# Performance work log

Hardware: AMD Instinct MI355X
Metric: run time of the kernel (lower is better)

## Reference

```python
import jax, jax.numpy as jnp
import numpy as np
from jax import lax

D_MODEL = 2048
D_STATE = 16
D_CONV = 4
B_SZ = 2
T_LEN = 2048


def setup_inputs() -> dict:
    key = jax.random.key(0)
    ks = jax.random.split(key, 8)
    x = jax.random.normal(ks[0], (B_SZ, T_LEN, D_MODEL), dtype=jnp.float32)
    h = jnp.zeros((B_SZ, D_MODEL, D_STATE), dtype=jnp.float32)
    norm_w = jnp.ones((D_MODEL,), dtype=jnp.float32)
    in_proj_w = jax.random.normal(ks[1], (2 * D_MODEL, D_MODEL), dtype=jnp.float32) * (D_MODEL ** -0.5)
    conv_w = jax.random.normal(ks[2], (D_MODEL, 1, D_CONV), dtype=jnp.float32) * 0.5
    conv_b = jnp.zeros((D_MODEL,), dtype=jnp.float32)
    x_proj_w = jax.random.normal(ks[3], (D_MODEL + 2 * D_STATE, D_MODEL), dtype=jnp.float32) * (D_MODEL ** -0.5)
    A_log = jnp.broadcast_to(jnp.log(jnp.arange(1, D_STATE + 1, dtype=jnp.float32))[None, :], (D_MODEL, D_STATE)).copy()
    D = jnp.ones((D_MODEL,), dtype=jnp.float32)
    out_proj_w = jax.random.normal(ks[4], (D_MODEL, D_MODEL), dtype=jnp.float32) * (D_MODEL ** -0.5)
    return {"x": x, "h": h, "norm_w": norm_w, "in_proj_w": in_proj_w,
            "conv_w": conv_w, "conv_b": conv_b, "x_proj_w": x_proj_w,
            "A_log": A_log, "D": D, "out_proj_w": out_proj_w}


def _rmsnorm(x, w, eps=1e-6):
    ms = jnp.mean(jnp.square(x.astype(jnp.float32)), axis=-1, keepdims=True)
    return (x * lax.rsqrt(ms + eps).astype(x.dtype)) * w.astype(x.dtype)


def reference(x, h, norm_w, in_proj_w, conv_w, conv_b, x_proj_w, A_log, D, out_proj_w):
    B, T, d_model = x.shape
    d_state = A_log.shape[1]
    residual = x
    x_normed = _rmsnorm(x, norm_w)
    xz = x_normed @ in_proj_w.T                      # (B, T, 2*d_model)
    x_branch, z = jnp.split(xz, 2, axis=-1)
    # depthwise causal conv1d: torch pads both sides by d_conv-1 then slices [:T],
    # equivalent to left-pad-only causal conv.
    xc = x_branch.transpose(0, 2, 1)                 # (B, d_model, T)
    xc = lax.conv_general_dilated(
        xc, conv_w, window_strides=(1,), padding=[(D_CONV - 1, 0)],
        dimension_numbers=("NCH", "OIH", "NCH"), feature_group_count=d_model)
    xc = xc + conv_b[None, :, None]
    x_ssm = jax.nn.silu(xc.transpose(0, 2, 1))       # (B, T, d_model)

    # SSM core
    proj = x_ssm @ x_proj_w.T                        # (B, T, d_model + 2*d_state)
    delta_raw = proj[..., :d_model]
    B_in = proj[..., d_model:d_model + d_state]
    C_in = proj[..., d_model + d_state:]
    delta = jax.nn.softplus(delta_raw)               # (B, T, d_model)
    A = -jnp.exp(A_log.astype(jnp.float32))          # (d_model, d_state)

    def step(h_c, inp):
        d_t, b_t, c_t, x_t = inp                     # (B,dm) (B,ds) (B,ds) (B,dm)
        A_bar = jnp.exp(d_t[:, :, None] * A[None])   # (B, dm, ds)
        h_c = A_bar * h_c + (d_t * x_t)[:, :, None] * b_t[:, None, :]
        y_t = jnp.einsum("bdn,bn->bd", h_c, c_t) + D * x_t
        return h_c, y_t

    xs = (delta.transpose(1, 0, 2), B_in.transpose(1, 0, 2),
          C_in.transpose(1, 0, 2), x_ssm.transpose(1, 0, 2))
    h_new, ys = lax.scan(step, h.astype(x.dtype), xs)
    y = ys.transpose(1, 0, 2)                        # (B, T, d_model)

    y = y * jax.nn.silu(z)
    out = residual + y @ out_proj_w.T
    return out, lax.stop_gradient(h_new)
```

## Files before the change

kernel.cpp:

```cpp
#include <hip/hip_runtime.h>
#include <cstdint>
#include <cstddef>


typedef __bf16 bf16_t;
typedef __attribute__((ext_vector_type(8))) __bf16 bf16x8;
typedef __attribute__((ext_vector_type(4))) __bf16 bf16x4;
typedef __attribute__((ext_vector_type(4))) float f32x4;

#define D_MODEL 2048
#define D_STATE 16
#define B_SZ 2
#define T_LEN 2048
#define N_ROWS (B_SZ * T_LEN)
#define N_PAD  2304
#define N_CHUNK 32
#define L_CHUNK (T_LEN / N_CHUNK)
#define LOG2E 1.4426950408889634f

__device__ __forceinline__ void load_lds16(const void* g, void* l) {
    __builtin_amdgcn_global_load_lds(
        (const __attribute__((address_space(1))) void*)(uintptr_t)g,
        (__attribute__((address_space(3))) void*)(uintptr_t)l,
        16, 0, 0);
}

#define VMW(n) asm volatile("s_waitcnt vmcnt(" #n ")" ::: "memory")
#define BAR()  do { __builtin_amdgcn_s_barrier(); __builtin_amdgcn_sched_barrier(0); } while (0)

__global__ __launch_bounds__(256) void cast_w13(
    const float* __restrict__ w1, const float* __restrict__ w3,
    bf16_t* __restrict__ d1, bf16_t* __restrict__ d3)
{
    int i = blockIdx.x * 256 + threadIdx.x;
    const int n1 = 4096 * 2048 / 4;
    if (i < n1) {
        f32x4 v = ((const f32x4*)w1)[i];
        ((bf16x4*)d1)[i] = __builtin_convertvector(v, bf16x4);
    } else {
        int j = i - n1;
        f32x4 v = ((const f32x4*)w3)[j];
        ((bf16x4*)d3)[j] = __builtin_convertvector(v, bf16x4);
    }
}

__global__ __launch_bounds__(256) void cast_pad_w2(
    const float* __restrict__ s, bf16_t* __restrict__ d)
{
    int i = blockIdx.x * 256 + threadIdx.x;
    int row = i >> 11;
    int col = i & 2047;
    float v = (row < 2080) ? s[(size_t)row * 2048 + col] : 0.f;
    d[i] = (bf16_t)v;
}

__global__ __launch_bounds__(256) void rmsnorm_kernel(
    const float* __restrict__ x, const float* __restrict__ w,
    bf16_t* __restrict__ xn)
{
    int row = blockIdx.x;
    int tid = threadIdx.x;
    const f32x4* xr = (const f32x4*)(x + (size_t)row * D_MODEL);
    f32x4 v0 = xr[tid];
    f32x4 v1 = xr[tid + 256];
    float ss = 0.f;
    #pragma unroll
    for (int e = 0; e < 4; ++e) { ss = fmaf(v0[e], v0[e], ss); ss = fmaf(v1[e], v1[e], ss); }
    #pragma unroll
    for (int o = 32; o > 0; o >>= 1) ss += __shfl_down(ss, o, 64);
    __shared__ float red[4];
    if ((tid & 63) == 0) red[tid >> 6] = ss;
    __syncthreads();
    float tot = red[0] + red[1] + red[2] + red[3];
    float scale = rsqrtf(tot * (1.f / D_MODEL) + 1e-6f);
    const f32x4* w4 = (const f32x4*)w;
    f32x4 m0 = v0 * w4[tid] * scale;
    f32x4 m1 = v1 * w4[tid + 256] * scale;
    bf16x4* xo = (bf16x4*)(xn + (size_t)row * D_MODEL);
    xo[tid]       = __builtin_convertvector(m0, bf16x4);
    xo[tid + 256] = __builtin_convertvector(m1, bf16x4);
}

template<int MODE>
__global__ __launch_bounds__(512, 2) void gemm_bt(
    const bf16_t* __restrict__ A, const bf16_t* __restrict__ Bw, int K,
    float* __restrict__ out0, bf16_t* __restrict__ out1,
    const float* __restrict__ add)
{
    __shared__ __align__(16) char smem[131072];
    char* const ldsAp = smem;
    char* const ldsBp = smem + 32768;

    const int tid  = threadIdx.x;
    const int nwg = gridDim.x * gridDim.y;
    const int lin = blockIdx.x + gridDim.x * blockIdx.y;
    const int wg  = (lin & 7) * (nwg >> 3) + (lin >> 3);
    const int bm  = wg & 15;
    const int bn  = wg >> 4;

    const int lane = tid & 63;
    const int wave = tid >> 6;
    const int wm   = wave >> 2;
    const int wn   = wave & 3;
    const int fr   = lane & 15;
    const int quad = lane >> 4;

    const int rS   = tid >> 2;
    const int cS   = tid & 3;
    const int gcol = ((cS - ((rS >> 1) & 3)) & 3) * 8;
    const bf16_t* pAg = A  + (size_t)(bm * 256 + rS) * K + gcol;
    const bf16_t* pBg = Bw + (size_t)(bn * 256 + rS) * K + gcol;

    const int swz  = ((quad + ((fr >> 1) & 3)) & 3) * 8;
    const int aOff = (wm * 128 + fr) * 32 + swz;
    const int bOff = (wn * 64  + fr) * 32 + swz;

    f32x4 acc[8][4];
    #pragma unroll
    for (int i = 0; i < 8; ++i)
        #pragma unroll
        for (int j = 0; j < 4; ++j) acc[i][j] = {0.f, 0.f, 0.f, 0.f};

    bf16x8 bfr[4];

#define STG_A(b, t, s) do { \
        const bf16_t* g_ = pAg + (t) * 64 + (s) * 32; \
        char* l_ = ldsAp + (b) * 65536 + (s) * 16384 + tid * 16; \
        load_lds16(g_, l_); load_lds16(g_ + (size_t)128 * K, l_ + 8192); } while (0)
#define STG_B(b, t, s) do { \
        const bf16_t* g_ = pBg + (t) * 64 + (s) * 32; \
        char* l_ = ldsBp + (b) * 65536 + (s) * 16384 + tid * 16; \
        load_lds16(g_, l_); load_lds16(g_ + (size_t)128 * K, l_ + 8192); } while (0)

#define PHASE(BUF, S, IH, STAGE_STMT, TAIL_STMT)                              \
    {                                                                         \
        const bf16_t* pA_ = (const bf16_t*)(ldsAp + (BUF)*65536 + (S)*16384); \
        if ((IH) == 0) {                                                      \
            const bf16_t* pB_ =                                               \
                (const bf16_t*)(ldsBp + (BUF)*65536 + (S)*16384);             \
            _Pragma("unroll")                                                 \
            for (int j = 0; j < 4; ++j)                                       \
                bfr[j] = *(const bf16x8*)(pB_ + bOff + j * 512);              \
        }                                                                     \
        bf16x8 af0 = *(const bf16x8*)(pA_ + aOff + ((IH)*4 + 0) * 512);       \
        bf16x8 af1 = *(const bf16x8*)(pA_ + aOff + ((IH)*4 + 1) * 512);       \
        bf16x8 af2 = *(const bf16x8*)(pA_ + aOff + ((IH)*4 + 2) * 512);       \
        bf16x8 af3 = *(const bf16x8*)(pA_ + aOff + ((IH)*4 + 3) * 512);       \
        STAGE_STMT;                                                           \
        BAR();                                                                \
        __builtin_amdgcn_s_setprio(1);                                        \
        _Pragma("unroll")                                                     \
        for (int j = 0; j < 4; ++j)                                           \
            acc[(IH)*4+0][j] = __builtin_amdgcn_mfma_f32_16x16x32_bf16(       \
                af0, bfr[j], acc[(IH)*4+0][j], 0, 0, 0);                      \
        _Pragma("unroll")                                                     \
        for (int j = 0; j < 4; ++j)                                           \
            acc[(IH)*4+1][j] = __builtin_amdgcn_mfma_f32_16x16x32_bf16(       \
                af1, bfr[j], acc[(IH)*4+1][j], 0, 0, 0);                      \
        _Pragma("unroll")                                                     \
        for (int j = 0; j < 4; ++j)                                           \
            acc[(IH)*4+2][j] = __builtin_amdgcn_mfma_f32_16x16x32_bf16(       \
                af2, bfr[j], acc[(IH)*4+2][j], 0, 0, 0);                      \
        _Pragma("unroll")                                                     \
        for (int j = 0; j < 4; ++j)                                           \
            acc[(IH)*4+3][j] = __builtin_amdgcn_mfma_f32_16x16x32_bf16(       \
                af3, bfr[j], acc[(IH)*4+3][j], 0, 0, 0);                      \
        __builtin_amdgcn_s_setprio(0);                                        \
        TAIL_STMT;                                                            \
        BAR();                                                                \
    }

    STG_B(0, 0, 0); STG_A(0, 0, 0); STG_B(0, 0, 1); STG_A(0, 0, 1);
    STG_B(1, 1, 0); STG_A(1, 1, 0); STG_B(1, 1, 1);
    VMW(10); BAR();

    const int NI = K >> 7;
    for (int I = 0; I < NI - 1; ++I) {
        const int t2 = 2 * I + 2, t3 = 2 * I + 3;
        PHASE(0, 0, 0, STG_A(1, t2 - 1, 1), (void)0)
        PHASE(0, 0, 1, STG_B(0, t2, 0),     VMW(10))
        PHASE(0, 1, 0, STG_A(0, t2, 0),     (void)0)
        PHASE(0, 1, 1, STG_B(0, t2, 1),     VMW(10))
        PHASE(1, 0, 0, STG_A(0, t2, 1),     (void)0)
        PHASE(1, 0, 1, STG_B(1, t3, 0),     VMW(10))
        PHASE(1, 1, 0, STG_A(1, t3, 0),     (void)0)
        PHASE(1, 1, 1, STG_B(1, t3, 1),     VMW(10))
    }
    PHASE(0, 0, 0, STG_A(1, 2 * NI - 1, 1), (void)0)
    PHASE(0, 0, 1, (void)0, VMW(8))
    PHASE(0, 1, 0, (void)0, (void)0)
    PHASE(0, 1, 1, (void)0, VMW(4))
    PHASE(1, 0, 0, (void)0, (void)0)
    PHASE(1, 0, 1, (void)0, VMW(0))
    PHASE(1, 1, 0, (void)0, (void)0)
    PHASE(1, 1, 1, (void)0, (void)0)
#undef STG_A
#undef STG_B
#undef PHASE

    float* const cs = (float*)smem;
    __syncthreads();
    #pragma unroll
    for (int s = 0; s < 4; ++s) {
        if (wm == (s >> 1)) {
            #pragma unroll
            for (int ii = 0; ii < 4; ++ii)
                #pragma unroll
                for (int j = 0; j < 4; ++j)
                    #pragma unroll
                    for (int rr = 0; rr < 4; ++rr)
                        cs[(ii * 16 + quad * 4 + rr) * 268 + wn * 64 + j * 16 + fr]
                            = acc[(s & 1) * 4 + ii][j][rr];
        }
        __syncthreads();
        #pragma unroll
        for (int k = 0; k < 8; ++k) {
            const int idx = tid + k * 512;
            const int row = idx >> 6;
            const int c4  = (idx & 63) << 2;
            f32x4 v = *(const f32x4*)(cs + row * 268 + c4);
            const int gr = bm * 256 + s * 64 + row;
            const int gc = bn * 256 + c4;
            if (MODE == 0) {
                if (bn < 8) {
                    *(f32x4*)&out0[(size_t)gr * 2048 + gc] = v;
                } else {
                    bf16x4 o;
                    #pragma unroll
                    for (int e = 0; e < 4; ++e) {
                        float sv = v[e];
                        o[e] = (bf16_t)(sv / (1.f + __expf(-sv)));
                    }
                    *(bf16x4*)&out1[(size_t)gr * 2048 + (gc - 2048)] = o;
                }
            } else if (MODE == 1) {
                if (bn < 8) {
                    #pragma unroll
                    for (int e = 0; e < 4; ++e) {
                        float sv = v[e];
                        v[e] = fmaxf(sv, 0.f) + __logf(1.f + __expf(-fabsf(sv)));
                    }
                }
                *(f32x4*)&out0[(size_t)gr * N_PAD + gc] = v;
            } else {
                f32x4 a4 = *(const f32x4*)&add[(size_t)gr * 2048 + gc];
                *(f32x4*)&out0[(size_t)gr * 2048 + gc] = v + a4;
            }
        }
        __syncthreads();
    }
}

__global__ __launch_bounds__(256) void conv_silu_kernel(
    const float* __restrict__ xb, const float* __restrict__ cw,
    const float* __restrict__ cb, bf16_t* __restrict__ xs_b)
{
    int id = blockIdx.x * 256 + threadIdx.x;
    int d  = id & 2047;
    int tb = (id >> 11) & 255;
    int b  = id >> 19;
    float w0 = cw[d * 4 + 0], w1 = cw[d * 4 + 1], w2 = cw[d * 4 + 2], w3 = cw[d * 4 + 3];
    float bias = cb[d];
    int t0 = tb * 8;
    size_t base = (size_t)b * T_LEN;
    float v[11];
    #pragma unroll
    for (int i = 0; i < 11; ++i) {
        int t = t0 - 3 + i;
        v[i] = (t >= 0) ? xb[(base + t) * 2048 + d] : 0.f;
    }
    #pragma unroll
    for (int j = 0; j < 8; ++j) {
        float s = bias + w0 * v[j] + w1 * v[j + 1] + w2 * v[j + 2] + w3 * v[j + 3];
        float sl = s / (1.f + __expf(-s));
        xs_b[(base + t0 + j) * D_MODEL + d] = (bf16_t)sl;
    }
}

#define PF 4

__global__ __launch_bounds__(256) void scan_phase1(
    const float* __restrict__ proj, const bf16_t* __restrict__ xs,
    const float* __restrict__ A_log,
    float* __restrict__ Aprod, float* __restrict__ hfin)
{
    int wi   = blockIdx.x * 4 + (threadIdx.x >> 6);
    int lane = threadIdx.x & 63;
    int nq   = lane & 3;
    int dsub = lane >> 2;
    int c  = wi & 31;
    int dg = (wi >> 5) & 127;
    int b  = wi >> 12;
    int dd = dg * 16 + dsub;

    float A2[4], h[4], Ap[4];
    #pragma unroll
    for (int j = 0; j < 4; ++j) {
        A2[j] = -__expf(A_log[dd * D_STATE + nq * 4 + j]) * LOG2E;
        h[j] = 0.f; Ap[j] = 1.f;
    }
    const int t0 = c * L_CHUNK;
    const int tmax = t0 + L_CHUNK - 1;

    float p_da[PF], p_xv[PF];
    f32x4 p_B[PF];
    #pragma unroll
    for (int u = 0; u < PF; ++u) {
        size_t row = (size_t)b * T_LEN + t0 + u;
        const float* pr = proj + row * N_PAD;
        p_da[u] = pr[dd];
        p_xv[u] = (float)xs[row * D_MODEL + dd];
        p_B[u]  = *(const f32x4*)(pr + D_MODEL + nq * 4);
    }

    for (int it = 0; it < L_CHUNK; it += PF) {
        #pragma unroll
        for (int u = 0; u < PF; ++u) {
            int t = t0 + it + u;
            float da = p_da[u], xv = p_xv[u];
            f32x4 Bv = p_B[u];
            int tn = t + PF; tn = (tn > tmax) ? tmax : tn;
            {
                size_t row = (size_t)b * T_LEN + tn;
                const float* pr = proj + row * N_PAD;
                p_da[u] = pr[dd];
                p_xv[u] = (float)xs[row * D_MODEL + dd];
                p_B[u]  = *(const f32x4*)(pr + D_MODEL + nq * 4);
            }
            float dx = da * xv;
            #pragma unroll
            for (int j = 0; j < 4; ++j) {
                float a = exp2f(da * A2[j]);
                Ap[j] *= a;
                h[j] = fmaf(a, h[j], dx * Bv[j]);
            }
        }
    }
    size_t o = ((size_t)c * 4096 + b * 2048 + dd) * D_STATE + nq * 4;
    *(f32x4*)(Aprod + o) = f32x4{Ap[0], Ap[1], Ap[2], Ap[3]};
    *(f32x4*)(hfin  + o) = f32x4{h[0], h[1], h[2], h[3]};
}

__global__ __launch_bounds__(256) void scan_phase2(
    const float* __restrict__ h_in, const float* __restrict__ Aprod,
    float* __restrict__ hfin, float* __restrict__ h_out)
{
    int g = blockIdx.x * 256 + threadIdx.x;
    float h = h_in[g];
    for (int c = 0; c < N_CHUNK; ++c) {
        size_t o = (size_t)c * 65536 + g;
        float a   = Aprod[o];
        float loc = hfin[o];
        hfin[o] = h;
        h = fmaf(a, h, loc);
    }
    h_out[g] = h;
}

__global__ __launch_bounds__(256) void scan_phase3(
    const float* __restrict__ proj, const bf16_t* __restrict__ xs,
    const bf16_t* __restrict__ zg, const float* __restrict__ A_log,
    const float* __restrict__ Dv, const float* __restrict__ hinit,
    bf16_t* __restrict__ yg)
{
    int wi   = blockIdx.x * 4 + (threadIdx.x >> 6);
    int lane = threadIdx.x & 63;
    int nq   = lane & 3;
    int dsub = lane >> 2;
    int c  = wi & 31;
    int dg = (wi >> 5) & 127;
    int b  = wi >> 12;
    int dd = dg * 16 + dsub;

    float A2[4], h[4];
    size_t o = ((size_t)c * 4096 + b * 2048 + dd) * D_STATE + nq * 4;
    #pragma unroll
    for (int j = 0; j < 4; ++j) {
        A2[j] = -__expf(A_log[dd * D_STATE + nq * 4 + j]) * LOG2E;
        h[j]  = hinit[o + j];
    }
    float Dd = Dv[dd];
    const int t0 = c * L_CHUNK;
    const int tmax = t0 + L_CHUNK - 1;

    float p_da[PF], p_xv[PF], p_sz[PF];
    f32x4 p_B[PF], p_C[PF];
    #pragma unroll
    for (int u = 0; u < PF; ++u) {
        size_t row = (size_t)b * T_LEN + t0 + u;
        const float* pr = proj + row * N_PAD;
        p_da[u] = pr[dd];
        p_xv[u] = (float)xs[row * D_MODEL + dd];
        p_sz[u] = (float)zg[row * 2048 + dd];
        p_B[u]  = *(const f32x4*)(pr + D_MODEL + nq * 4);
        p_C[u]  = *(const f32x4*)(pr + D_MODEL + D_STATE + nq * 4);
    }

    for (int it = 0; it < L_CHUNK; it += PF) {
        #pragma unroll
        for (int u = 0; u < PF; ++u) {
            int t = t0 + it + u;
            float da = p_da[u], xv = p_xv[u], sz = p_sz[u];
            f32x4 Bv = p_B[u], Cv = p_C[u];
            int tn = t + PF; tn = (tn > tmax) ? tmax : tn;
            {
                size_t row = (size_t)b * T_LEN + tn;
                const float* pr = proj + row * N_PAD;
                p_da[u] = pr[dd];
                p_xv[u] = (float)xs[row * D_MODEL + dd];
                p_sz[u] = (float)zg[row * 2048 + dd];
                p_B[u]  = *(const f32x4*)(pr + D_MODEL + nq * 4);
                p_C[u]  = *(const f32x4*)(pr + D_MODEL + D_STATE + nq * 4);
            }
            float dx = da * xv;
            float yp = 0.f;
            #pragma unroll
            for (int j = 0; j < 4; ++j) {
                float a = exp2f(da * A2[j]);
                h[j] = fmaf(a, h[j], dx * Bv[j]);
                yp = fmaf(h[j], Cv[j], yp);
            }
            yp += __shfl_xor(yp, 1, 64);
            yp += __shfl_xor(yp, 2, 64);
            if (nq == 0) {
                float y = fmaf(Dd, xv, yp);
                yg[((size_t)b * T_LEN + t) * D_MODEL + dd] = (bf16_t)(y * sz);
            }
        }
    }
}

extern "C" void kernel_launch(void* const* d_in, const int* in_sizes, int n_in,
                              void* d_out, int out_size, void* d_ws, size_t ws_size,
                              hipStream_t stream)
{
    const float* x    = (const float*)d_in[0];
    const float* h0   = (const float*)d_in[1];
    const float* nw   = (const float*)d_in[2];
    const float* w_in = (const float*)d_in[3];
    const float* cw   = (const float*)d_in[4];
    const float* cb   = (const float*)d_in[5];
    const float* w_x  = (const float*)d_in[6];
    const float* alog = (const float*)d_in[7];
    const float* dv   = (const float*)d_in[8];
    const float* w_out= (const float*)d_in[9];
    float* out  = (float*)d_out;
    float* hout = out + (size_t)N_ROWS * D_MODEL;

    char* ws = (char*)d_ws;
    size_t off = 0;
    auto alloc = [&](size_t bytes) -> void* {
        void* p = ws + off;
        off += (bytes + 255) & ~(size_t)255;
        return p;
    };
    bf16_t* W1  = (bf16_t*)alloc((size_t)4096 * 2048 * 2);
    bf16_t* W2  = (bf16_t*)alloc((size_t)N_PAD * 2048 * 2);
    bf16_t* W3  = (bf16_t*)alloc((size_t)2048 * 2048 * 2);
    bf16_t* XN  = (bf16_t*)alloc((size_t)N_ROWS * 2048 * 2);
    float*  XB  = (float*) alloc((size_t)N_ROWS * 2048 * 4);
    bf16_t* ZG  = (bf16_t*)alloc((size_t)N_ROWS * 2048 * 2);
    float*  PROJ= (float*) alloc((size_t)N_ROWS * N_PAD * 4);
    float* APROD= (float*) alloc((size_t)N_CHUNK * 4096 * D_STATE * 4);
    float* HFIN = (float*) alloc((size_t)N_CHUNK * 4096 * D_STATE * 4);
    bf16_t* XSb = W1;
    bf16_t* YG  = XN;

    cast_w13<<<(4096 * 2048 / 4 + 2048 * 2048 / 4) / 256, 256, 0, stream>>>(w_in, w_out, W1, W3);
    cast_pad_w2<<<(N_PAD * 2048) / 256, 256, 0, stream>>>(w_x, W2);

    rmsnorm_kernel<<<N_ROWS, 256, 0, stream>>>(x, nw, XN);
    gemm_bt<0><<<dim3(16, 16), 512, 0, stream>>>(XN, W1, 2048, XB, ZG, nullptr);
    conv_silu_kernel<<<(B_SZ * (T_LEN / 8) * D_MODEL) / 256, 256, 0, stream>>>(XB, cw, cb, XSb);
    gemm_bt<1><<<dim3(16, N_PAD / 256), 512, 0, stream>>>(XSb, W2, 2048, PROJ, nullptr, nullptr);
    scan_phase1<<<2048, 256, 0, stream>>>(PROJ, XSb, alog, APROD, HFIN);
    scan_phase2<<<256, 256, 0, stream>>>(h0, APROD, HFIN, hout);
    scan_phase3<<<2048, 256, 0, stream>>>(PROJ, XSb, ZG, alog, dv, HFIN, YG);
    gemm_bt<2><<<dim3(16, 8), 512, 0, stream>>>(YG, W3, 2048, out, nullptr, x);

    (void)in_sizes; (void)n_in; (void)out_size; (void)ws_size;
}
```

Measured before the change: 470.0 us.

## Loosen GEMM pipeline waits, drop sched barriers, use running global pointers

```diff
diff --git a/kernel.cpp b/kernel.cpp
--- a/kernel.cpp
+++ b/kernel.cpp
@@ -26,7 +26,8 @@
 }
 
 #define VMW(n) asm volatile("s_waitcnt vmcnt(" #n ")" ::: "memory")
-#define BAR()  do { __builtin_amdgcn_s_barrier(); __builtin_amdgcn_sched_barrier(0); } while (0)
+#define BARP() __builtin_amdgcn_s_barrier()
+#define BARG() do { __builtin_amdgcn_s_barrier(); __builtin_amdgcn_sched_barrier(0); } while (0)
 
 __global__ __launch_bounds__(256) void cast_w13(
     const float* __restrict__ w1, const float* __restrict__ w3,
@@ -108,8 +109,8 @@
     const int rS   = tid >> 2;
     const int cS   = tid & 3;
     const int gcol = ((cS - ((rS >> 1) & 3)) & 3) * 8;
-    const bf16_t* pAg = A  + (size_t)(bm * 256 + rS) * K + gcol;
-    const bf16_t* pBg = Bw + (size_t)(bn * 256 + rS) * K + gcol;
+    const bf16_t* sAn = A  + (size_t)(bm * 256 + rS) * K + gcol;
+    const bf16_t* sBn = Bw + (size_t)(bn * 256 + rS) * K + gcol;
 
     const int swz  = ((quad + ((fr >> 1) & 3)) & 3) * 8;
     const int aOff = (wm * 128 + fr) * 32 + swz;
@@ -123,16 +124,16 @@
 
     bf16x8 bfr[4];
 
-#define STG_A(b, t, s) do { \
-        const bf16_t* g_ = pAg + (t) * 64 + (s) * 32; \
+#define STG_A(b, s) do { \
         char* l_ = ldsAp + (b) * 65536 + (s) * 16384 + tid * 16; \
-        load_lds16(g_, l_); load_lds16(g_ + (size_t)128 * K, l_ + 8192); } while (0)
-#define STG_B(b, t, s) do { \
-        const bf16_t* g_ = pBg + (t) * 64 + (s) * 32; \
+        load_lds16(sAn, l_); load_lds16(sAn + (size_t)128 * K, l_ + 8192); \
+        sAn += 32; } while (0)
+#define STG_B(b, s) do { \
         char* l_ = ldsBp + (b) * 65536 + (s) * 16384 + tid * 16; \
-        load_lds16(g_, l_); load_lds16(g_ + (size_t)128 * K, l_ + 8192); } while (0)
-
-#define PHASE(BUF, S, IH, STAGE_STMT, TAIL_STMT)                              \
+        load_lds16(sBn, l_); load_lds16(sBn + (size_t)128 * K, l_ + 8192); \
+        sBn += 32; } while (0)
+
+#define PHASE(BUF, S, IH, STAGE_STMT, TAIL_STMT, CLOSE)                       \
     {                                                                         \
         const bf16_t* pA_ = (const bf16_t*)(ldsAp + (BUF)*65536 + (S)*16384); \
         if ((IH) == 0) {                                                      \
@@ -147,7 +148,7 @@
         bf16x8 af2 = *(const bf16x8*)(pA_ + aOff + ((IH)*4 + 2) * 512);       \
         bf16x8 af3 = *(const bf16x8*)(pA_ + aOff + ((IH)*4 + 3) * 512);       \
         STAGE_STMT;                                                           \
-        BAR();                                                                \
+        BARP();                                                               \
         __builtin_amdgcn_s_setprio(1);                                        \
         _Pragma("unroll")                                                     \
         for (int j = 0; j < 4; ++j)                                           \
@@ -167,33 +168,32 @@
                 af3, bfr[j], acc[(IH)*4+3][j], 0, 0, 0);                      \
         __builtin_amdgcn_s_setprio(0);                                        \
         TAIL_STMT;                                                            \
-        BAR();                                                                \
-    }
-
-    STG_B(0, 0, 0); STG_A(0, 0, 0); STG_B(0, 0, 1); STG_A(0, 0, 1);
-    STG_B(1, 1, 0); STG_A(1, 1, 0); STG_B(1, 1, 1);
-    VMW(10); BAR();
+        CLOSE();                                                              \
+    }
+
+    STG_B(0, 0); STG_A(0, 0); STG_B(0, 1); STG_A(0, 1);
+    STG_B(1, 0); STG_A(1, 0); STG_B(1, 1);
+    VMW(6); BARG();
 
     const int NI = K >> 7;
     for (int I = 0; I < NI - 1; ++I) {
-        const int t2 = 2 * I + 2, t3 = 2 * I + 3;
-        PHASE(0, 0, 0, STG_A(1, t2 - 1, 1), (void)0)
-        PHASE(0, 0, 1, STG_B(0, t2, 0),     VMW(10))
-        PHASE(0, 1, 0, STG_A(0, t2, 0),     (void)0)
-        PHASE(0, 1, 1, STG_B(0, t2, 1),     VMW(10))
-        PHASE(1, 0, 0, STG_A(0, t2, 1),     (void)0)
-        PHASE(1, 0, 1, STG_B(1, t3, 0),     VMW(10))
-        PHASE(1, 1, 0, STG_A(1, t3, 0),     (void)0)
-        PHASE(1, 1, 1, STG_B(1, t3, 1),     VMW(10))
-    }
-    PHASE(0, 0, 0, STG_A(1, 2 * NI - 1, 1), (void)0)
-    PHASE(0, 0, 1, (void)0, VMW(8))
-    PHASE(0, 1, 0, (void)0, (void)0)
-    PHASE(0, 1, 1, (void)0, VMW(4))
-    PHASE(1, 0, 0, (void)0, (void)0)
-    PHASE(1, 0, 1, (void)0, VMW(0))
-    PHASE(1, 1, 0, (void)0, (void)0)
-    PHASE(1, 1, 1, (void)0, (void)0)
+        PHASE(0, 0, 0, STG_A(1, 1), (void)0, BARP)
+        PHASE(0, 0, 1, STG_B(0, 0), (void)0, BARP)
+        PHASE(0, 1, 0, STG_A(0, 0), (void)0, BARP)
+        PHASE(0, 1, 1, STG_B(0, 1), VMW(6),  BARG)
+        PHASE(1, 0, 0, STG_A(0, 1), (void)0, BARP)
+        PHASE(1, 0, 1, STG_B(1, 0), (void)0, BARP)
+        PHASE(1, 1, 0, STG_A(1, 0), (void)0, BARP)
+        PHASE(1, 1, 1, STG_B(1, 1), VMW(6),  BARG)
+    }
+    PHASE(0, 0, 0, STG_A(1, 1), (void)0, BARP)
+    PHASE(0, 0, 1, (void)0,     (void)0, BARP)
+    PHASE(0, 1, 0, (void)0,     (void)0, BARP)
+    PHASE(0, 1, 1, (void)0,     VMW(0),  BARG)
+    PHASE(1, 0, 0, (void)0,     (void)0, BARP)
+    PHASE(1, 0, 1, (void)0,     (void)0, BARP)
+    PHASE(1, 1, 0, (void)0,     (void)0, BARP)
+    PHASE(1, 1, 1, (void)0,     (void)0, BARP)
 #undef STG_A
 #undef STG_B
 #undef PHASE
```

Result: no change. 475.9 us (+1.3%).
